# Performance work log

Measured on AMD Instinct MI355X. Metric: run time of the kernel, lower is better.

Reference implementation:

```python
import jax, jax.numpy as jnp
import numpy as np

N, E, B, D, R, L = 60000, 600000, 512, 128, 30, 3
CUT_LOW, CUT_HIGH = 0.0, 10.0
N_ATOM_TYPES = 100


def _sp(x, beta, threshold):
    # torch.nn.Softplus(beta, threshold): x if beta*x > threshold else log1p(exp(beta*x))/beta
    bx = beta * x
    return jnp.where(bx > threshold, x, jnp.log1p(jnp.exp(jnp.minimum(bx, threshold))) / beta)


def setup_inputs() -> dict:
    key = jax.random.key(0)
    ks = jax.random.split(key, 16)

    def lin(k, fi, fo):
        k1, k2 = jax.random.split(k)
        W = jax.random.normal(k1, (fi, fo), jnp.float32) * (fi ** -0.5)
        b = jax.random.normal(k2, (fo,), jnp.float32) * 0.01
        return W, b

    def lin_stack(k, fi, fo, n):
        Ws, bs = zip(*[lin(kk, fi, fo) for kk in jax.random.split(k, n)])
        return jnp.stack(Ws), jnp.stack(bs)

    inp = {}
    inp['atom_type'] = jax.random.randint(ks[0], (N,), 0, N_ATOM_TYPES)
    inp['src'] = jax.random.randint(ks[1], (E,), 0, N)
    inp['dst'] = jax.random.randint(ks[2], (E,), 0, N)
    inp['graph_ids'] = jnp.sort(jax.random.randint(ks[3], (N,), 0, B))
    inp['dist'] = jax.random.uniform(ks[4], (E,), jnp.float32) * CUT_HIGH
    inp['node_emb'] = jax.random.normal(ks[5], (N_ATOM_TYPES, D), jnp.float32) * 0.1
    inp['W_n1'], inp['b_n1'] = lin_stack(ks[6], D, D, L)
    inp['W_c1'], inp['b_c1'] = lin_stack(ks[7], R, D, L)
    inp['W_c2'], inp['b_c2'] = lin_stack(ks[8], D, D, L)
    inp['W_c3'], inp['b_c3'] = lin_stack(ks[9], D, D, L)
    inp['W_n2'], inp['b_n2'] = lin_stack(ks[10], D, D, L)
    inp['W_n3'], inp['b_n3'] = lin_stack(ks[11], D, D, L)
    inp['W_r1'], inp['b_r1'] = lin(ks[12], D * (L + 1), 64)
    inp['W_r2'], inp['b_r2'] = lin(ks[13], 64, 1)
    return inp


def reference(atom_type, src, dst, graph_ids, dist, node_emb,
              W_n1, b_n1, W_c1, b_c1, W_c2, b_c2, W_c3, b_c3,
              W_n2, b_n2, W_n3, b_n3, W_r1, b_r1, W_r2, b_r2):
    # RBF expansion of edge distances: exp(-(d - mu_k)^2 / gap)  -> [E, R]
    centers = jnp.linspace(CUT_LOW, CUT_HIGH, R).astype(dist.dtype)
    gap = centers[1] - centers[0]
    rbf = jnp.exp(-((dist[:, None] - centers) ** 2) / gap)

    h = node_emb[atom_type]  # node embedding lookup [N, D]
    hs = [h]
    for i in range(L):  # MultiLevelInteraction layers (fixed small count)
        h_new = hs[-1] @ W_n1[i] + b_n1[i]                       # node_layer1 [N, D]
        # VEConv edge MLP on rbf (linear1 -> softplus(0.5,14) -> linear2 -> linear3)
        e = _sp(rbf @ W_c1[i] + b_c1[i], 0.5, 14.0) @ W_c2[i] + b_c2[i]
        e = e @ W_c3[i] + b_c3[i]                                 # [E, D]
        # sum_e(h_new[src]*e) + sum_e(e) fused into one scatter-sum over dst
        msg = (h_new[src] + 1.0) * e                              # [E, D]
        node = jax.ops.segment_sum(msg, dst, num_segments=N)      # [N, D]
        new_node = _sp(node @ W_n2[i] + b_n2[i], 0.5, 14.0) @ W_n3[i] + b_n3[i]
        hs.append(hs[-1] + new_node)                              # residual h_i
    hcat = jnp.concatenate(hs, axis=1)                            # [N, D*(L+1)]
    out = _sp(hcat @ W_r1 + b_r1, 1.0, 20.0) @ W_r2 + b_r2        # [N, 1]
    # dgl.sum_nodes per molecule, then flatten -> [B]
    return jax.ops.segment_sum(out[:, 0], graph_ids, num_segments=B)
```

## Files before the change

### kernel.cpp

```cpp
#include <hip/hip_runtime.h>
#include <math.h>

#define N_NODES 60000
#define N_EDGES 600000
#define B_GRAPHS 512
#define DIM 128
#define RBF_R 30
#define NLAYERS 3
#define NBINS 1024
#define CHUNK 512
#define NCHUNK ((N_NODES + CHUNK - 1) / CHUNK)

typedef __attribute__((ext_vector_type(8))) short bf16x8;
typedef __attribute__((ext_vector_type(4))) float f32x4;

__device__ __forceinline__ float sp05(float x) {
    float bx = 0.5f * x;
    return bx > 14.0f ? x : 2.0f * log1pf(expf(bx));
}
__device__ __forceinline__ float sp1(float x) {
    return x > 20.0f ? x : log1pf(expf(x));
}
__device__ __forceinline__ unsigned short f2bf(float f) {
    unsigned int u = __float_as_uint(f);
    unsigned int r = u + 0x7FFFu + ((u >> 16) & 1u);
    return (unsigned short)(r >> 16);
}
__device__ __forceinline__ float bf2f(unsigned int s) {
    return __uint_as_float(s << 16);
}


__global__ void k_convW(const float* __restrict__ Wn1, const float* __restrict__ Wn2,
                        const float* __restrict__ Wn3, unsigned short* __restrict__ WtF) {
    int i = blockIdx.x * 256 + threadIdx.x;
    int mat = i >> 14, r = i & 16383;
    int frag = r >> 9, within = r & 511;
    int ks = frag >> 3, ntile = frag & 7;
    int lane = within >> 3, j = within & 7;
    int q = lane >> 4, l16 = lane & 15;
    int n = ntile * 16 + l16;
    int k = ks * 32 + q * 8 + j;
    const float* src = (mat < 3) ? (Wn1 + (size_t)mat * 16384)
                     : (mat < 6) ? (Wn2 + (size_t)(mat - 3) * 16384)
                                 : (Wn3 + (size_t)(mat - 6) * 16384);
    WtF[i] = f2bf(src[k * 128 + n]);
}

__global__ void k_convR(const float* __restrict__ Wr1, unsigned short* __restrict__ Wr1tF) {
    int i = blockIdx.x * 256 + threadIdx.x;
    int frag = i >> 9, within = i & 511;
    int lvl = frag >> 4, ks = (frag >> 2) & 3, ntile = frag & 3;
    int lane = within >> 3, j = within & 7;
    int q = lane >> 4, l16 = lane & 15;
    int n = ntile * 16 + l16;
    int k = lvl * 128 + ks * 32 + q * 8 + j;
    Wr1tF[i] = f2bf(Wr1[k * 64 + n]);
}

__global__ void k_embed(const int* __restrict__ atom_type,
                        const float* __restrict__ node_emb,
                        float* __restrict__ h0, unsigned short* __restrict__ hb0) {
    int i = blockIdx.x * blockDim.x + threadIdx.x;
    if (i >= N_NODES * DIM) return;
    int n = i >> 7, d = i & 127;
    float v = node_emb[atom_type[n] * DIM + d];
    h0[i] = v;
    hb0[i] = f2bf(v);
}


__global__ void k_hist(const int* __restrict__ dst, int* __restrict__ counts) {
    int e = blockIdx.x * blockDim.x + threadIdx.x;
    if (e >= N_EDGES) return;
    atomicAdd(&counts[dst[e]], 1);
}

__global__ void k_bsum(const int* __restrict__ counts, int* __restrict__ bsums) {
    __shared__ int red[256];
    int c = blockIdx.x, tid = threadIdx.x;
    int base = c * CHUNK;
    int v = 0;
    for (int i = tid; i < CHUNK; i += 256)
        if (base + i < N_NODES) v += counts[base + i];
    red[tid] = v;
    __syncthreads();
    for (int s = 128; s > 0; s >>= 1) {
        if (tid < s) red[tid] += red[tid + s];
        __syncthreads();
    }
    if (tid == 0) bsums[c] = red[0];
}

__global__ void k_scan_b(int* __restrict__ bsums) {
    __shared__ int sb[NCHUNK];
    int tid = threadIdx.x;
    if (tid < NCHUNK) sb[tid] = bsums[tid];
    __syncthreads();
    if (tid == 0) {
        int run = 0;
        for (int i = 0; i < NCHUNK; ++i) { int v = sb[i]; sb[i] = run; run += v; }
    }
    __syncthreads();
    if (tid < NCHUNK) bsums[tid] = sb[tid];
}

__global__ void k_scan_final(const int* __restrict__ counts, const int* __restrict__ bsums,
                             int* __restrict__ offsets) {
    __shared__ int sc[CHUNK];
    int c = blockIdx.x, tid = threadIdx.x;
    int base = c * CHUNK;
    for (int i = tid; i < CHUNK; i += 256)
        sc[i] = (base + i < N_NODES) ? counts[base + i] : 0;
    __syncthreads();
    if (tid == 0) {
        int run = bsums[c];
        for (int i = 0; i < CHUNK; ++i) { int v = sc[i]; sc[i] = run; run += v; }
    }
    __syncthreads();
    for (int i = tid; i < CHUNK; i += 256)
        if (base + i < N_NODES) offsets[base + i] = sc[i];
    if (c == 0 && tid == 0) offsets[N_NODES] = N_EDGES;
}

__global__ void k_fill(const int* __restrict__ src, const int* __restrict__ dst,
                       const float* __restrict__ dist,
                       const int* __restrict__ offsets, int* __restrict__ cnt2,
                       uint2* __restrict__ meta) {
    int e = blockIdx.x * blockDim.x + threadIdx.x;
    if (e >= N_EDGES) return;
    int d = dst[e];
    int pos = offsets[d] + atomicAdd(&cnt2[d], 1);
    float x = dist[e];
    float p = x * ((float)NBINS / 10.0f);
    int bin = (int)p;
    if (bin > NBINS - 1) bin = NBINS - 1;
    float w = p - (float)bin;
    int wq = (int)(w * 65535.0f + 0.5f);
    if (wq > 65535) wq = 65535;
    meta[pos] = make_uint2((unsigned)src[e], ((unsigned)bin << 16) | (unsigned)wq);
}


__global__ void k_table(const float* __restrict__ Wc1, const float* __restrict__ bc1,
                        const float* __restrict__ Wc2, const float* __restrict__ bc2,
                        const float* __restrict__ Wc3, const float* __restrict__ bc3,
                        unsigned short* __restrict__ tableb) {
    __shared__ float t[DIM];
    __shared__ float u[DIM];
    int b = blockIdx.x;
    int d = threadIdx.x;
    float dist = (float)b * (10.0f / (float)NBINS);
    const float gap = 10.0f / 29.0f;
    float acc = bc1[d];
#pragma unroll
    for (int k = 0; k < RBF_R; ++k) {
        float c = (float)k * (10.0f / 29.0f);
        float df = dist - c;
        acc += expf(-df * df / gap) * Wc1[k * DIM + d];
    }
    t[d] = sp05(acc);
    __syncthreads();
    acc = bc2[d];
#pragma unroll 8
    for (int k = 0; k < DIM; ++k) acc += t[k] * Wc2[k * DIM + d];
    u[d] = acc;
    __syncthreads();
    acc = bc3[d];
#pragma unroll 8
    for (int k = 0; k < DIM; ++k) acc += u[k] * Wc3[k * DIM + d];
    tableb[b * DIM + d] = f2bf(acc);
}

__global__ void k_pack(const unsigned short* __restrict__ tableb,
                       unsigned int* __restrict__ packed) {
    int i = blockIdx.x * 256 + threadIdx.x;
    float a = bf2f(tableb[i]);
    float b = bf2f(tableb[i + DIM]);
    packed[i] = (unsigned int)f2bf(a) | ((unsigned int)f2bf(b - a) << 16);
}

__global__ __launch_bounds__(256) void k_gemm_g(const unsigned short* __restrict__ Ab,
                                                const unsigned short* __restrict__ WtF,
                                                const float* __restrict__ bias,
                                                unsigned short* __restrict__ Cb) {
    int tid = threadIdx.x;
    int wave = tid >> 6, lane = tid & 63;
    int q = lane >> 4, l16 = lane & 15;
    int mhalf = wave & 1, nhalf = wave >> 1;
    int rb = blockIdx.x * 64 + mhalf * 32;
    int c0 = nhalf * 64;
    bf16x8 bfrag[4][4];
#pragma unroll
    for (int ks = 0; ks < 4; ++ks)
#pragma unroll
        for (int nt = 0; nt < 4; ++nt)
            bfrag[ks][nt] = *(const bf16x8*)&WtF[(size_t)(ks * 8 + nhalf * 4 + nt) * 512 + lane * 8];
    f32x4 acc[2][4] = {};
#pragma unroll
    for (int ks = 0; ks < 4; ++ks)
#pragma unroll
        for (int mt = 0; mt < 2; ++mt) {
            int m = rb + mt * 16 + l16;
            if (m > N_NODES - 1) m = N_NODES - 1;
            bf16x8 a = *(const bf16x8*)&Ab[(size_t)m * 128 + ks * 32 + q * 8];
#pragma unroll
            for (int nt = 0; nt < 4; ++nt)
                acc[mt][nt] = __builtin_amdgcn_mfma_f32_16x16x32_bf16(a, bfrag[ks][nt], acc[mt][nt], 0, 0, 0);
        }
#pragma unroll
    for (int mt = 0; mt < 2; ++mt)
#pragma unroll
        for (int nt = 0; nt < 4; ++nt) {
            int col = c0 + nt * 16 + l16;
            float b = bias[col] + 1.0f;
#pragma unroll
            for (int r = 0; r < 4; ++r) {
                int row = rb + mt * 16 + q * 4 + r;
                if (row < N_NODES) Cb[(size_t)row * 128 + col] = f2bf(acc[mt][nt][r] + b);
            }
        }
}

__global__ __launch_bounds__(256) void k_gather(
    const int* __restrict__ offsets, const uint2* __restrict__ meta,
    const unsigned int* __restrict__ packed, const unsigned short* __restrict__ gb,
    unsigned short* __restrict__ nodeb) {
    int wave = threadIdx.x >> 6, lane = threadIdx.x & 63;
    int n = blockIdx.x * 4 + wave;
    int beg = offsets[n], end = offsets[n + 1];
    int off = lane * 2;
    const float ws = 1.0f / 65535.0f;
    float acc0 = 0.f, acc1 = 0.f, acc2 = 0.f, acc3 = 0.f;
    int j = beg;
    for (; j + 4 <= end; j += 4) {
        uint2 m0 = meta[j], m1 = meta[j + 1], m2 = meta[j + 2], m3 = meta[j + 3];
        uint2 p0 = *(const uint2*)&packed[(size_t)(m0.y >> 16) * DIM + off];
        uint2 p1 = *(const uint2*)&packed[(size_t)(m1.y >> 16) * DIM + off];
        uint2 p2 = *(const uint2*)&packed[(size_t)(m2.y >> 16) * DIM + off];
        uint2 p3 = *(const uint2*)&packed[(size_t)(m3.y >> 16) * DIM + off];
        unsigned int g0 = *(const unsigned int*)&gb[(size_t)m0.x * DIM + off];
        unsigned int g1 = *(const unsigned int*)&gb[(size_t)m1.x * DIM + off];
        unsigned int g2 = *(const unsigned int*)&gb[(size_t)m2.x * DIM + off];
        unsigned int g3 = *(const unsigned int*)&gb[(size_t)m3.x * DIM + off];
        float w0 = (float)(m0.y & 0xffff) * ws;
        float w1 = (float)(m1.y & 0xffff) * ws;
        float w2 = (float)(m2.y & 0xffff) * ws;
        float w3 = (float)(m3.y & 0xffff) * ws;
        acc0 += bf2f(g0 & 0xffff) * (bf2f(p0.x & 0xffff) + w0 * bf2f(p0.x >> 16));
        acc1 += bf2f(g0 >> 16)    * (bf2f(p0.y & 0xffff) + w0 * bf2f(p0.y >> 16));
        acc2 += bf2f(g1 & 0xffff) * (bf2f(p1.x & 0xffff) + w1 * bf2f(p1.x >> 16));
        acc3 += bf2f(g1 >> 16)    * (bf2f(p1.y & 0xffff) + w1 * bf2f(p1.y >> 16));
        acc0 += bf2f(g2 & 0xffff) * (bf2f(p2.x & 0xffff) + w2 * bf2f(p2.x >> 16));
        acc1 += bf2f(g2 >> 16)    * (bf2f(p2.y & 0xffff) + w2 * bf2f(p2.y >> 16));
        acc2 += bf2f(g3 & 0xffff) * (bf2f(p3.x & 0xffff) + w3 * bf2f(p3.x >> 16));
        acc3 += bf2f(g3 >> 16)    * (bf2f(p3.y & 0xffff) + w3 * bf2f(p3.y >> 16));
    }
    for (; j < end; ++j) {
        uint2 m0 = meta[j];
        uint2 p0 = *(const uint2*)&packed[(size_t)(m0.y >> 16) * DIM + off];
        unsigned int g0 = *(const unsigned int*)&gb[(size_t)m0.x * DIM + off];
        float w0 = (float)(m0.y & 0xffff) * ws;
        acc0 += bf2f(g0 & 0xffff) * (bf2f(p0.x & 0xffff) + w0 * bf2f(p0.x >> 16));
        acc1 += bf2f(g0 >> 16)    * (bf2f(p0.y & 0xffff) + w0 * bf2f(p0.y >> 16));
    }
    acc0 += acc2; acc1 += acc3;
    unsigned int o = (unsigned int)f2bf(acc0) | ((unsigned int)f2bf(acc1) << 16);
    *(unsigned int*)&nodeb[(size_t)n * DIM + off] = o;
}

__global__ __launch_bounds__(256) void k_node_update(
    const unsigned short* __restrict__ nodeb,
    const unsigned short* __restrict__ W2tF, const float* __restrict__ b2,
    const unsigned short* __restrict__ W3tF, const float* __restrict__ b3,
    const float* __restrict__ h_in, float* __restrict__ h_out,
    unsigned short* __restrict__ hb_out) {
    __shared__ unsigned short ts[64][136];
    int tid = threadIdx.x;
    int wave = tid >> 6, lane = tid & 63;
    int q = lane >> 4, l16 = lane & 15;
    int mhalf = wave & 1, nhalf = wave >> 1;
    int rb = blockIdx.x * 64 + mhalf * 32;
    int c0 = nhalf * 64;

    bf16x8 bfrag[4][4];
#pragma unroll
    for (int ks = 0; ks < 4; ++ks)
#pragma unroll
        for (int nt = 0; nt < 4; ++nt)
            bfrag[ks][nt] = *(const bf16x8*)&W2tF[(size_t)(ks * 8 + nhalf * 4 + nt) * 512 + lane * 8];
    f32x4 acc[2][4] = {};
#pragma unroll
    for (int ks = 0; ks < 4; ++ks)
#pragma unroll
        for (int mt = 0; mt < 2; ++mt) {
            int m = rb + mt * 16 + l16;
            if (m > N_NODES - 1) m = N_NODES - 1;
            bf16x8 a = *(const bf16x8*)&nodeb[(size_t)m * 128 + ks * 32 + q * 8];
#pragma unroll
            for (int nt = 0; nt < 4; ++nt)
                acc[mt][nt] = __builtin_amdgcn_mfma_f32_16x16x32_bf16(a, bfrag[ks][nt], acc[mt][nt], 0, 0, 0);
        }
#pragma unroll
    for (int mt = 0; mt < 2; ++mt)
#pragma unroll
        for (int nt = 0; nt < 4; ++nt) {
            int col = c0 + nt * 16 + l16;
            float b = b2[col];
#pragma unroll
            for (int r = 0; r < 4; ++r) {
                int lrow = mhalf * 32 + mt * 16 + q * 4 + r;
                ts[lrow][col] = f2bf(sp05(acc[mt][nt][r] + b));
            }
        }
    __syncthreads();
#pragma unroll
    for (int ks = 0; ks < 4; ++ks)
#pragma unroll
        for (int nt = 0; nt < 4; ++nt)
            bfrag[ks][nt] = *(const bf16x8*)&W3tF[(size_t)(ks * 8 + nhalf * 4 + nt) * 512 + lane * 8];
#pragma unroll
    for (int mt = 0; mt < 2; ++mt)
#pragma unroll
        for (int nt = 0; nt < 4; ++nt) acc[mt][nt] = (f32x4){0.f, 0.f, 0.f, 0.f};
#pragma unroll
    for (int ks = 0; ks < 4; ++ks)
#pragma unroll
        for (int mt = 0; mt < 2; ++mt) {
            int lrow = mhalf * 32 + mt * 16 + l16;
            bf16x8 a = *(const bf16x8*)&ts[lrow][ks * 32 + q * 8];
#pragma unroll
            for (int nt = 0; nt < 4; ++nt)
                acc[mt][nt] = __builtin_amdgcn_mfma_f32_16x16x32_bf16(a, bfrag[ks][nt], acc[mt][nt], 0, 0, 0);
        }
#pragma unroll
    for (int mt = 0; mt < 2; ++mt)
#pragma unroll
        for (int nt = 0; nt < 4; ++nt) {
            int col = c0 + nt * 16 + l16;
            float b = b3[col];
#pragma unroll
            for (int r = 0; r < 4; ++r) {
                int row = rb + mt * 16 + q * 4 + r;
                if (row < N_NODES) {
                    size_t idx = (size_t)row * 128 + col;
                    float v = h_in[idx] + acc[mt][nt][r] + b;
                    h_out[idx] = v;
                    hb_out[idx] = f2bf(v);
                }
            }
        }
}

__global__ __launch_bounds__(256) void k_readout(
    const unsigned short* __restrict__ hb0, const unsigned short* __restrict__ hb1,
    const unsigned short* __restrict__ hb2, const unsigned short* __restrict__ hb3,
    const unsigned short* __restrict__ Wr1tF, const float* __restrict__ br1,
    const float* __restrict__ Wr2, const float* __restrict__ br2,
    const int* __restrict__ graph_ids, float* __restrict__ out) {
    __shared__ uint4 sB4[4096];
    int tid = threadIdx.x;
    const uint4* wsrc = (const uint4*)Wr1tF;
    for (int i = tid; i < 4096; i += 256) sB4[i] = wsrc[i];
    __syncthreads();
    const unsigned short* sB = (const unsigned short*)sB4;
    int wave = tid >> 6, lane = tid & 63;
    int q = lane >> 4, l16 = lane & 15;
    int rb0 = blockIdx.x * 128 + wave * 16;
    const unsigned short* hbs[4] = {hb0, hb1, hb2, hb3};
    f32x4 acc[2][4] = {};
    for (int lvl = 0; lvl < 4; ++lvl) {
        bf16x8 bf[4][4];
#pragma unroll
        for (int ks = 0; ks < 4; ++ks)
#pragma unroll
            for (int nt = 0; nt < 4; ++nt)
                bf[ks][nt] = *(const bf16x8*)&sB[(size_t)((lvl * 4 + ks) * 4 + nt) * 512 + lane * 8];
        const unsigned short* Ab = hbs[lvl];
        bf16x8 a[2][4];
#pragma unroll
        for (int mt = 0; mt < 2; ++mt)
#pragma unroll
            for (int ks = 0; ks < 4; ++ks) {
                int m = rb0 + mt * 64 + l16;
                if (m > N_NODES - 1) m = N_NODES - 1;
                a[mt][ks] = *(const bf16x8*)&Ab[(size_t)m * 128 + ks * 32 + q * 8];
            }
#pragma unroll
        for (int ks = 0; ks < 4; ++ks)
#pragma unroll
            for (int mt = 0; mt < 2; ++mt)
#pragma unroll
                for (int nt = 0; nt < 4; ++nt)
                    acc[mt][nt] = __builtin_amdgcn_mfma_f32_16x16x32_bf16(a[mt][ks], bf[ks][nt], acc[mt][nt], 0, 0, 0);
    }
    float brr = br2[0];
#pragma unroll
    for (int mt = 0; mt < 2; ++mt) {
        float partial[4] = {0.f, 0.f, 0.f, 0.f};
#pragma unroll
        for (int nt = 0; nt < 4; ++nt) {
            int col = nt * 16 + l16;
            float b = br1[col];
            float w = Wr2[col];
#pragma unroll
            for (int r = 0; r < 4; ++r) partial[r] += sp1(acc[mt][nt][r] + b) * w;
        }
#pragma unroll
        for (int r = 0; r < 4; ++r) {
            float v = partial[r];
            v += __shfl_xor(v, 1); v += __shfl_xor(v, 2);
            v += __shfl_xor(v, 4); v += __shfl_xor(v, 8);
            if (l16 == 0) {
                int row = rb0 + mt * 64 + q * 4 + r;
                if (row < N_NODES) atomicAdd(&out[graph_ids[row]], v + brr);
            }
        }
    }
}

extern "C" void kernel_launch(void* const* d_in, const int* in_sizes, int n_in,
                              void* d_out, int out_size, void* d_ws, size_t ws_size,
                              hipStream_t stream) {
    const int* atom_type   = (const int*)d_in[0];
    const int* src         = (const int*)d_in[1];
    const int* dst         = (const int*)d_in[2];
    const int* graph_ids   = (const int*)d_in[3];
    const float* dist      = (const float*)d_in[4];
    const float* node_emb  = (const float*)d_in[5];
    const float* W_n1 = (const float*)d_in[6];  const float* b_n1 = (const float*)d_in[7];
    const float* W_c1 = (const float*)d_in[8];  const float* b_c1 = (const float*)d_in[9];
    const float* W_c2 = (const float*)d_in[10]; const float* b_c2 = (const float*)d_in[11];
    const float* W_c3 = (const float*)d_in[12]; const float* b_c3 = (const float*)d_in[13];
    const float* W_n2 = (const float*)d_in[14]; const float* b_n2 = (const float*)d_in[15];
    const float* W_n3 = (const float*)d_in[16]; const float* b_n3 = (const float*)d_in[17];
    const float* W_r1 = (const float*)d_in[18]; const float* b_r1 = (const float*)d_in[19];
    const float* W_r2 = (const float*)d_in[20]; const float* b_r2 = (const float*)d_in[21];
    float* out = (float*)d_out;

    size_t ND = (size_t)N_NODES * DIM;
    float* h_even = (float*)d_ws;
    float* h_odd  = h_even + ND;
    uint2* meta   = (uint2*)(h_odd + ND);
    int* offsets  = (int*)(meta + N_EDGES);
    int* counts   = offsets + 60008;
    int* cnt2     = counts + N_NODES;
    int* bsums    = cnt2 + N_NODES;
    unsigned int* packed = (unsigned int*)(bsums + 128);
    unsigned short* hb0    = (unsigned short*)(packed + (size_t)NBINS * DIM);
    unsigned short* hb1    = hb0 + ND;
    unsigned short* hb2    = hb1 + ND;
    unsigned short* hb3    = hb2 + ND;
    unsigned short* gb     = hb3 + ND;
    unsigned short* nodeb  = gb + ND;
    unsigned short* tableb = nodeb + ND;
    unsigned short* WtF    = tableb + (size_t)(NBINS + 1) * DIM;
    unsigned short* Wr1tF  = WtF + 9 * 16384;

    unsigned short* hbp[4] = {hb0, hb1, hb2, hb3};
    float* hcur = h_even;
    float* hnext = h_odd;

    hipMemsetAsync(out, 0, B_GRAPHS * sizeof(float), stream);
    hipMemsetAsync(counts, 0, (2 * N_NODES + 128) * sizeof(int), stream);

    k_convW<<<(9 * 16384) / 256, 256, 0, stream>>>(W_n1, W_n2, W_n3, WtF);
    k_convR<<<32768 / 256, 256, 0, stream>>>(W_r1, Wr1tF);
    k_embed<<<(N_NODES * DIM) / 256, 256, 0, stream>>>(atom_type, node_emb, h_even, hb0);

    k_hist<<<(N_EDGES + 255) / 256, 256, 0, stream>>>(dst, counts);
    k_bsum<<<NCHUNK, 256, 0, stream>>>(counts, bsums);
    k_scan_b<<<1, 128, 0, stream>>>(bsums);
    k_scan_final<<<NCHUNK, 256, 0, stream>>>(counts, bsums, offsets);
    k_fill<<<(N_EDGES + 255) / 256, 256, 0, stream>>>(src, dst, dist, offsets, cnt2, meta);

    int gblocks = (N_NODES + 63) / 64;
    int rblocks = (N_NODES + 127) / 128;
    for (int i = 0; i < NLAYERS; ++i) {
        k_table<<<NBINS + 1, DIM, 0, stream>>>(
            W_c1 + (size_t)i * RBF_R * DIM, b_c1 + (size_t)i * DIM,
            W_c2 + (size_t)i * DIM * DIM,  b_c2 + (size_t)i * DIM,
            W_c3 + (size_t)i * DIM * DIM,  b_c3 + (size_t)i * DIM, tableb);
        k_pack<<<(NBINS * DIM) / 256, 256, 0, stream>>>(tableb, packed);
        k_gemm_g<<<gblocks, 256, 0, stream>>>(
            hbp[i], WtF + (size_t)i * 16384, b_n1 + (size_t)i * DIM, gb);
        k_gather<<<N_NODES / 4, 256, 0, stream>>>(offsets, meta, packed, gb, nodeb);
        k_node_update<<<gblocks, 256, 0, stream>>>(
            nodeb, WtF + (size_t)(3 + i) * 16384, b_n2 + (size_t)i * DIM,
            WtF + (size_t)(6 + i) * 16384, b_n3 + (size_t)i * DIM,
            hcur, hnext, hbp[i + 1]);
        float* tmp = hcur; hcur = hnext; hnext = tmp;
    }
    k_readout<<<rblocks, 256, 0, stream>>>(
        hb0, hb1, hb2, hb3, Wr1tF, b_r1, W_r2, b_r2, graph_ids, out);
}
```

Before: 640.7 us.

## Merge setup kernels, batch per-layer tables, single-block scan, readout weights from global

Fuses the two weight-conversion kernels into one launch, replaces the three-kernel offset scan with a single 1024-thread block scan, and builds the edge-filter lookup tables for all three layers in one launch before the layer loop instead of per layer. The readout kernel now reads its weight fragments directly from global memory instead of staging them in shared memory, and issues MFMAs as each A fragment is loaded. The goal is fewer kernel launches and serial dependencies. In exchange it uses more workspace for the three tables, and the readout's global weight reads may cost more than the old shared-memory staging.

```diff
diff --git a/kernel.cpp b/kernel.cpp
--- a/kernel.cpp
+++ b/kernel.cpp
@@ -8,8 +8,6 @@
 #define RBF_R 30
 #define NLAYERS 3
 #define NBINS 1024
-#define CHUNK 512
-#define NCHUNK ((N_NODES + CHUNK - 1) / CHUNK)
 
 typedef __attribute__((ext_vector_type(8))) short bf16x8;
 typedef __attribute__((ext_vector_type(4))) float f32x4;
@@ -30,32 +28,34 @@
     return __uint_as_float(s << 16);
 }
 
-
-__global__ void k_convW(const float* __restrict__ Wn1, const float* __restrict__ Wn2,
-                        const float* __restrict__ Wn3, unsigned short* __restrict__ WtF) {
+__global__ void k_conv(const float* __restrict__ Wn1, const float* __restrict__ Wn2,
+                       const float* __restrict__ Wn3, const float* __restrict__ Wr1,
+                       unsigned short* __restrict__ WtF, unsigned short* __restrict__ Wr1tF) {
     int i = blockIdx.x * 256 + threadIdx.x;
-    int mat = i >> 14, r = i & 16383;
-    int frag = r >> 9, within = r & 511;
-    int ks = frag >> 3, ntile = frag & 7;
-    int lane = within >> 3, j = within & 7;
-    int q = lane >> 4, l16 = lane & 15;
-    int n = ntile * 16 + l16;
-    int k = ks * 32 + q * 8 + j;
-    const float* src = (mat < 3) ? (Wn1 + (size_t)mat * 16384)
-                     : (mat < 6) ? (Wn2 + (size_t)(mat - 3) * 16384)
-                                 : (Wn3 + (size_t)(mat - 6) * 16384);
-    WtF[i] = f2bf(src[k * 128 + n]);
-}
-
-__global__ void k_convR(const float* __restrict__ Wr1, unsigned short* __restrict__ Wr1tF) {
-    int i = blockIdx.x * 256 + threadIdx.x;
-    int frag = i >> 9, within = i & 511;
-    int lvl = frag >> 4, ks = (frag >> 2) & 3, ntile = frag & 3;
-    int lane = within >> 3, j = within & 7;
-    int q = lane >> 4, l16 = lane & 15;
-    int n = ntile * 16 + l16;
-    int k = lvl * 128 + ks * 32 + q * 8 + j;
-    Wr1tF[i] = f2bf(Wr1[k * 64 + n]);
+    if (i < 9 * 16384) {
+        int mat = i >> 14, r = i & 16383;
+        int frag = r >> 9, within = r & 511;
+        int ks = frag >> 3, ntile = frag & 7;
+        int lane = within >> 3, j = within & 7;
+        int q = lane >> 4, l16 = lane & 15;
+        int n = ntile * 16 + l16;
+        int k = ks * 32 + q * 8 + j;
+        const float* src = (mat < 3) ? (Wn1 + (size_t)mat * 16384)
+                         : (mat < 6) ? (Wn2 + (size_t)(mat - 3) * 16384)
+                                     : (Wn3 + (size_t)(mat - 6) * 16384);
+        WtF[i] = f2bf(src[k * 128 + n]);
+    } else {
+        int ii = i - 9 * 16384;
+        if (ii < 32768) {
+            int frag = ii >> 9, within = ii & 511;
+            int lvl = frag >> 4, ks = (frag >> 2) & 3, ntile = frag & 3;
+            int lane = within >> 3, j = within & 7;
+            int q = lane >> 4, l16 = lane & 15;
+            int n = ntile * 16 + l16;
+            int k = lvl * 128 + ks * 32 + q * 8 + j;
+            Wr1tF[ii] = f2bf(Wr1[k * 64 + n]);
+        }
+    }
 }
 
 __global__ void k_embed(const int* __restrict__ atom_type,
@@ -76,51 +76,31 @@
     atomicAdd(&counts[dst[e]], 1);
 }
 
-__global__ void k_bsum(const int* __restrict__ counts, int* __restrict__ bsums) {
-    __shared__ int red[256];
-    int c = blockIdx.x, tid = threadIdx.x;
-    int base = c * CHUNK;
-    int v = 0;
-    for (int i = tid; i < CHUNK; i += 256)
-        if (base + i < N_NODES) v += counts[base + i];
-    red[tid] = v;
+__global__ void k_scan_all(const int* __restrict__ counts, int* __restrict__ offsets) {
+    __shared__ int sums[1024];
+    int tid = threadIdx.x;
+    const int CPT = 60;
+    int base = tid * CPT;
+    int s = 0;
+#pragma unroll 4
+    for (int i = 0; i < CPT; ++i) {
+        int idx = base + i;
+        if (idx < N_NODES) s += counts[idx];
+    }
+    sums[tid] = s;
     __syncthreads();
-    for (int s = 128; s > 0; s >>= 1) {
-        if (tid < s) red[tid] += red[tid + s];
+    for (int off = 1; off < 1024; off <<= 1) {
+        int v = (tid >= off) ? sums[tid - off] : 0;
         __syncthreads();
-    }
-    if (tid == 0) bsums[c] = red[0];
-}
-
-__global__ void k_scan_b(int* __restrict__ bsums) {
-    __shared__ int sb[NCHUNK];
-    int tid = threadIdx.x;
-    if (tid < NCHUNK) sb[tid] = bsums[tid];
-    __syncthreads();
-    if (tid == 0) {
-        int run = 0;
-        for (int i = 0; i < NCHUNK; ++i) { int v = sb[i]; sb[i] = run; run += v; }
-    }
-    __syncthreads();
-    if (tid < NCHUNK) bsums[tid] = sb[tid];
-}
-
-__global__ void k_scan_final(const int* __restrict__ counts, const int* __restrict__ bsums,
-                             int* __restrict__ offsets) {
-    __shared__ int sc[CHUNK];
-    int c = blockIdx.x, tid = threadIdx.x;
-    int base = c * CHUNK;
-    for (int i = tid; i < CHUNK; i += 256)
-        sc[i] = (base + i < N_NODES) ? counts[base + i] : 0;
-    __syncthreads();
-    if (tid == 0) {
-        int run = bsums[c];
-        for (int i = 0; i < CHUNK; ++i) { int v = sc[i]; sc[i] = run; run += v; }
-    }
-    __syncthreads();
-    for (int i = tid; i < CHUNK; i += 256)
-        if (base + i < N_NODES) offsets[base + i] = sc[i];
-    if (c == 0 && tid == 0) offsets[N_NODES] = N_EDGES;
+        sums[tid] += v;
+        __syncthreads();
+    }
+    int run = (tid == 0) ? 0 : sums[tid - 1];
+    for (int i = 0; i < CPT; ++i) {
+        int idx = base + i;
+        if (idx < N_NODES) { int c = counts[idx]; offsets[idx] = run; run += c; }
+    }
+    if (tid == 1023) offsets[N_NODES] = N_EDGES;
 }
 
 __global__ void k_fill(const int* __restrict__ src, const int* __restrict__ dst,
@@ -142,43 +122,51 @@
 }
 
 
-__global__ void k_table(const float* __restrict__ Wc1, const float* __restrict__ bc1,
-                        const float* __restrict__ Wc2, const float* __restrict__ bc2,
-                        const float* __restrict__ Wc3, const float* __restrict__ bc3,
-                        unsigned short* __restrict__ tableb) {
+__global__ void k_table_all(const float* __restrict__ Wc1, const float* __restrict__ bc1,
+                            const float* __restrict__ Wc2, const float* __restrict__ bc2,
+                            const float* __restrict__ Wc3, const float* __restrict__ bc3,
+                            unsigned short* __restrict__ tableb) {
     __shared__ float t[DIM];
     __shared__ float u[DIM];
-    int b = blockIdx.x;
+    int lyr = blockIdx.x / (NBINS + 1);
+    int b = blockIdx.x % (NBINS + 1);
     int d = threadIdx.x;
+    const float* wc1 = Wc1 + (size_t)lyr * RBF_R * DIM;
+    const float* wc2 = Wc2 + (size_t)lyr * DIM * DIM;
+    const float* wc3 = Wc3 + (size_t)lyr * DIM * DIM;
     float dist = (float)b * (10.0f / (float)NBINS);
     const float gap = 10.0f / 29.0f;
-    float acc = bc1[d];
+    float acc = bc1[lyr * DIM + d];
 #pragma unroll
     for (int k = 0; k < RBF_R; ++k) {
         float c = (float)k * (10.0f / 29.0f);
         float df = dist - c;
-        acc += expf(-df * df / gap) * Wc1[k * DIM + d];
+        acc += expf(-df * df / gap) * wc1[k * DIM + d];
     }
     t[d] = sp05(acc);
     __syncthreads();
-    acc = bc2[d];
+    acc = bc2[lyr * DIM + d];
 #pragma unroll 8
-    for (int k = 0; k < DIM; ++k) acc += t[k] * Wc2[k * DIM + d];
+    for (int k = 0; k < DIM; ++k) acc += t[k] * wc2[k * DIM + d];
     u[d] = acc;
     __syncthreads();
-    acc = bc3[d];
+    acc = bc3[lyr * DIM + d];
 #pragma unroll 8
-    for (int k = 0; k < DIM; ++k) acc += u[k] * Wc3[k * DIM + d];
-    tableb[b * DIM + d] = f2bf(acc);
-}
-
-__global__ void k_pack(const unsigned short* __restrict__ tableb,
-                       unsigned int* __restrict__ packed) {
+    for (int k = 0; k < DIM; ++k) acc += u[k] * wc3[k * DIM + d];
+    tableb[((size_t)lyr * (NBINS + 1) + b) * DIM + d] = f2bf(acc);
+}
+
+__global__ void k_pack_all(const unsigned short* __restrict__ tableb,
+                           unsigned int* __restrict__ packed) {
     int i = blockIdx.x * 256 + threadIdx.x;
-    float a = bf2f(tableb[i]);
-    float b = bf2f(tableb[i + DIM]);
+    int lyr = i / (NBINS * DIM);
+    int r = i % (NBINS * DIM);
+    const unsigned short* tb = tableb + (size_t)lyr * (NBINS + 1) * DIM;
+    float a = bf2f(tb[r]);
+    float b = bf2f(tb[r + DIM]);
     packed[i] = (unsigned int)f2bf(a) | ((unsigned int)f2bf(b - a) << 16);
 }
+
 
 __global__ __launch_bounds__(256) void k_gemm_g(const unsigned short* __restrict__ Ab,
                                                 const unsigned short* __restrict__ WtF,
@@ -358,41 +346,31 @@
     const unsigned short* __restrict__ Wr1tF, const float* __restrict__ br1,
     const float* __restrict__ Wr2, const float* __restrict__ br2,
     const int* __restrict__ graph_ids, float* __restrict__ out) {
-    __shared__ uint4 sB4[4096];
     int tid = threadIdx.x;
-    const uint4* wsrc = (const uint4*)Wr1tF;
-    for (int i = tid; i < 4096; i += 256) sB4[i] = wsrc[i];
-    __syncthreads();
-    const unsigned short* sB = (const unsigned short*)sB4;
     int wave = tid >> 6, lane = tid & 63;
     int q = lane >> 4, l16 = lane & 15;
     int rb0 = blockIdx.x * 128 + wave * 16;
     const unsigned short* hbs[4] = {hb0, hb1, hb2, hb3};
     f32x4 acc[2][4] = {};
     for (int lvl = 0; lvl < 4; ++lvl) {
-        bf16x8 bf[4][4];
+        bf16x8 bfrag[4][4];
 #pragma unroll
         for (int ks = 0; ks < 4; ++ks)
 #pragma unroll
             for (int nt = 0; nt < 4; ++nt)
-                bf[ks][nt] = *(const bf16x8*)&sB[(size_t)((lvl * 4 + ks) * 4 + nt) * 512 + lane * 8];
+                bfrag[ks][nt] = *(const bf16x8*)&Wr1tF[(size_t)((lvl * 4 + ks) * 4 + nt) * 512 + lane * 8];
         const unsigned short* Ab = hbs[lvl];
-        bf16x8 a[2][4];
-#pragma unroll
-        for (int mt = 0; mt < 2; ++mt)
-#pragma unroll
-            for (int ks = 0; ks < 4; ++ks) {
+#pragma unroll
+        for (int ks = 0; ks < 4; ++ks)
+#pragma unroll
+            for (int mt = 0; mt < 2; ++mt) {
                 int m = rb0 + mt * 64 + l16;
                 if (m > N_NODES - 1) m = N_NODES - 1;
-                a[mt][ks] = *(const bf16x8*)&Ab[(size_t)m * 128 + ks * 32 + q * 8];
+                bf16x8 a = *(const bf16x8*)&Ab[(size_t)m * 128 + ks * 32 + q * 8];
+#pragma unroll
+                for (int nt = 0; nt < 4; ++nt)
+                    acc[mt][nt] = __builtin_amdgcn_mfma_f32_16x16x32_bf16(a, bfrag[ks][nt], acc[mt][nt], 0, 0, 0);
             }
-#pragma unroll
-        for (int ks = 0; ks < 4; ++ks)
-#pragma unroll
-            for (int mt = 0; mt < 2; ++mt)
-#pragma unroll
-                for (int nt = 0; nt < 4; ++nt)
-                    acc[mt][nt] = __builtin_amdgcn_mfma_f32_16x16x32_bf16(a[mt][ks], bf[ks][nt], acc[mt][nt], 0, 0, 0);
     }
     float brr = br2[0];
 #pragma unroll
@@ -445,16 +423,15 @@
     int* offsets  = (int*)(meta + N_EDGES);
     int* counts   = offsets + 60008;
     int* cnt2     = counts + N_NODES;
-    int* bsums    = cnt2 + N_NODES;
-    unsigned int* packed = (unsigned int*)(bsums + 128);
-    unsigned short* hb0    = (unsigned short*)(packed + (size_t)NBINS * DIM);
+    unsigned int* packed = (unsigned int*)(cnt2 + N_NODES);
+    unsigned short* hb0    = (unsigned short*)(packed + (size_t)3 * NBINS * DIM);
     unsigned short* hb1    = hb0 + ND;
     unsigned short* hb2    = hb1 + ND;
     unsigned short* hb3    = hb2 + ND;
     unsigned short* gb     = hb3 + ND;
     unsigned short* nodeb  = gb + ND;
     unsigned short* tableb = nodeb + ND;
-    unsigned short* WtF    = tableb + (size_t)(NBINS + 1) * DIM;
+    unsigned short* WtF    = tableb + (size_t)3 * (NBINS + 1) * DIM;
     unsigned short* Wr1tF  = WtF + 9 * 16384;
 
     unsigned short* hbp[4] = {hb0, hb1, hb2, hb3};
@@ -462,29 +439,26 @@
     float* hnext = h_odd;
 
     hipMemsetAsync(out, 0, B_GRAPHS * sizeof(float), stream);
-    hipMemsetAsync(counts, 0, (2 * N_NODES + 128) * sizeof(int), stream);
-
-    k_convW<<<(9 * 16384) / 256, 256, 0, stream>>>(W_n1, W_n2, W_n3, WtF);
-    k_convR<<<32768 / 256, 256, 0, stream>>>(W_r1, Wr1tF);
+    hipMemsetAsync(counts, 0, 2 * N_NODES * sizeof(int), stream);
+
+    k_conv<<<(9 * 16384 + 32768 + 255) / 256, 256, 0, stream>>>(
+        W_n1, W_n2, W_n3, W_r1, WtF, Wr1tF);
     k_embed<<<(N_NODES * DIM) / 256, 256, 0, stream>>>(atom_type, node_emb, h_even, hb0);
+    k_table_all<<<3 * (NBINS + 1), DIM, 0, stream>>>(
+        W_c1, b_c1, W_c2, b_c2, W_c3, b_c3, tableb);
+    k_pack_all<<<(3 * NBINS * DIM) / 256, 256, 0, stream>>>(tableb, packed);
 
     k_hist<<<(N_EDGES + 255) / 256, 256, 0, stream>>>(dst, counts);
-    k_bsum<<<NCHUNK, 256, 0, stream>>>(counts, bsums);
-    k_scan_b<<<1, 128, 0, stream>>>(bsums);
-    k_scan_final<<<NCHUNK, 256, 0, stream>>>(counts, bsums, offsets);
+    k_scan_all<<<1, 1024, 0, stream>>>(counts, offsets);
     k_fill<<<(N_EDGES + 255) / 256, 256, 0, stream>>>(src, dst, dist, offsets, cnt2, meta);
 
     int gblocks = (N_NODES + 63) / 64;
     int rblocks = (N_NODES + 127) / 128;
     for (int i = 0; i < NLAYERS; ++i) {
-        k_table<<<NBINS + 1, DIM, 0, stream>>>(
-            W_c1 + (size_t)i * RBF_R * DIM, b_c1 + (size_t)i * DIM,
-            W_c2 + (size_t)i * DIM * DIM,  b_c2 + (size_t)i * DIM,
-            W_c3 + (size_t)i * DIM * DIM,  b_c3 + (size_t)i * DIM, tableb);
-        k_pack<<<(NBINS * DIM) / 256, 256, 0, stream>>>(tableb, packed);
         k_gemm_g<<<gblocks, 256, 0, stream>>>(
             hbp[i], WtF + (size_t)i * 16384, b_n1 + (size_t)i * DIM, gb);
-        k_gather<<<N_NODES / 4, 256, 0, stream>>>(offsets, meta, packed, gb, nodeb);
+        k_gather<<<N_NODES / 4, 256, 0, stream>>>(
+            offsets, meta, packed + (size_t)i * NBINS * DIM, gb, nodeb);
         k_node_update<<<gblocks, 256, 0, stream>>>(
             nodeb, WtF + (size_t)(3 + i) * 16384, b_n2 + (size_t)i * DIM,
             WtF + (size_t)(6 + i) * 16384, b_n3 + (size_t)i * DIM,
```

Measured after the change: 679.4 us. 6.0% more time.
